# Kernel tuning notes

Measured on AMD Instinct MI355X. Metric: run time of the kernel, lower is better.

Reference implementation:

```python
import jax, jax.numpy as jnp
import numpy as np
import math

STEM = 64
TOK = 128
RADIUS = 0.16
K = 32


def sinusoidal_pos_emb_3d(x, dim):
    # x: [..., 3] -> [..., dim]; dim/3 channels per axis (half sin, half cos)
    per_axis = dim // 3
    half = per_axis // 2
    scale = math.log(10000.0) / (half - 1)
    freqs = jnp.exp(-scale * jnp.arange(half, dtype=x.dtype))  # [half]
    ang = x[..., :, None] * freqs  # [..., 3, half]
    emb = jnp.concatenate([jnp.sin(ang), jnp.cos(ang)], axis=-1)  # [..., 3, per_axis]
    return emb.reshape(*x.shape[:-1], dim)


def query_ball_point(radius, nsample, xyz):
    # xyz: [B, N, 3] -> idx [B, N, nsample] int32
    B, N, _ = xyz.shape
    d2 = jnp.sum((xyz[:, :, None, :] - xyz[:, None, :, :]) ** 2, axis=-1)  # [B,N,N]
    cand = jnp.where(d2 <= radius * radius, jnp.arange(N, dtype=jnp.int32)[None, None, :], N)
    idx = jnp.sort(cand, axis=-1)[..., :nsample]  # first nsample in-ball indices
    first = idx[..., :1]  # self is always in-ball (d=0), so first is valid
    return jnp.where(idx == N, first, idx)


def index_points(points, idx):
    # points [B,N,C], idx [B,S,K] -> [B,S,K,C]
    return jax.vmap(lambda p, i: p[i])(points, idx)


def point_mlp(x, W, b, activate):
    y = x @ W + b
    return jax.nn.relu(y) if activate else y


def setup_inputs() -> dict:
    key = jax.random.key(0)
    ks = jax.random.split(key, 10)
    B, N = 2, 4096
    xyz = jax.random.uniform(ks[0], (B, N, 3), dtype=jnp.float32)
    point_feature = jax.random.normal(ks[1], (B, N, STEM), dtype=jnp.float32)
    c_in = STEM + 3 + 24 + 96  # 187
    def lin(k, i, o):
        s = 1.0 / np.sqrt(i)
        return jax.random.uniform(k, (i, o), jnp.float32, -s, s)
    W1 = lin(ks[2], c_in, TOK); b1 = jnp.zeros((TOK,), jnp.float32)
    W2 = lin(ks[3], TOK, TOK); b2 = jnp.zeros((TOK,), jnp.float32)
    W3 = lin(ks[4], TOK, TOK); b3 = jnp.zeros((TOK,), jnp.float32)
    W4 = lin(ks[5], TOK, TOK); b4 = jnp.zeros((TOK,), jnp.float32)
    return {"xyz": xyz, "point_feature": point_feature,
            "W1": W1, "b1": b1, "W2": W2, "b2": b2,
            "W3": W3, "b3": b3, "W4": W4, "b4": b4}


def reference(xyz, point_feature, W1, b1, W2, b2, W3, b3, W4, b4):
    idx = query_ball_point(RADIUS, K, xyz)                 # [B,N,K]
    grouped_xyz = index_points(xyz, idx)                   # [B,N,K,3]
    grouped_feature = index_points(point_feature, idx)     # [B,N,K,STEM]
    relative_xyz = grouped_xyz - xyz[:, :, None, :]        # [B,N,K,3]
    rel_pe = sinusoidal_pos_emb_3d(relative_xyz, 24)       # [B,N,K,24]
    abs_pe = sinusoidal_pos_emb_3d(xyz, 96)                # [B,N,96]
    abs_pe = jnp.broadcast_to(abs_pe[:, :, None, :], (*idx.shape, 96))
    grouped_input = jnp.concatenate(
        [grouped_feature, relative_xyz, rel_pe, abs_pe], axis=-1)  # [B,N,K,187]
    h = point_mlp(grouped_input, W1, b1, True)
    h = point_mlp(h, W2, b2, False)                        # [B,N,K,TOK]
    scene_point_feature = jnp.max(h, axis=2)               # [B,N,TOK]
    g = jnp.max(scene_point_feature, axis=1, keepdims=True)  # [B,1,TOK]
    g = point_mlp(g, W3, b3, True)
    return point_mlp(g, W4, b4, False)                     # [B,1,TOK]
```

## Files before the change

kernel.cpp:

```cpp
#include <hip/hip_runtime.h>
#include <stdint.h>

#define BATCH 2
#define NPTS  4096
#define KNBR  32
#define TOKC  128

typedef _Float16 half8 __attribute__((ext_vector_type(8)));
typedef _Float16 half4 __attribute__((ext_vector_type(4)));
typedef float    f32x4 __attribute__((ext_vector_type(4)));

#define OFF_FH    (1u << 20)
#define OFF_AH    (3u << 20)
#define OFF_W1F   ((5u << 20) + 2048)
#define OFF_W2F   ((5u << 20) + 10240)
#define OFF_BMAX  (6u << 20)
#define OFF_BMAX2 (7u << 20)
#define OFF_CNT   ((7u << 20) + 32768)

#define NMAIN 1024

__global__ __launch_bounds__(256) void k_pre(const float* __restrict__ xyz,
                                             const float* __restrict__ feat,
                                             const float* __restrict__ W1,
                                             const float* __restrict__ W2,
                                             const float* __restrict__ b1,
                                             int* __restrict__ oidx,
                                             _Float16* __restrict__ Fh,
                                             _Float16* __restrict__ Ah,
                                             _Float16* __restrict__ W1F,
                                             _Float16* __restrict__ W2F,
                                             unsigned int* __restrict__ cntp) {
    __shared__ __align__(16) _Float16 inL[16][168];
    const int t = threadIdx.x;
    const int w = t >> 6, lane = t & 63;

    if (blockIdx.x < 2048) {
        int wave = blockIdx.x * 4 + w;
        int b = wave >> 12;
        int n = wave & (NPTS - 1);
        const float* xb = xyz + (size_t)b * NPTS * 3;
        float cx = xb[n * 3 + 0], cy = xb[n * 3 + 1], cz = xb[n * 3 + 2];
        const float R2 = 0.0256f;
        int cnt = 0;
        int first = 0;
        int* out = oidx + (size_t)wave * KNBR;
        float cur[12], nxt[12];
        #pragma unroll
        for (int u = 0; u < 4; u++) {
            int j = u * 64 + lane;
            cur[u * 3 + 0] = xb[j * 3 + 0];
            cur[u * 3 + 1] = xb[j * 3 + 1];
            cur[u * 3 + 2] = xb[j * 3 + 2];
        }
        for (int base = 0; base < NPTS; base += 256) {
            #pragma clang fp contract(off)
            if (base + 256 < NPTS) {
                #pragma unroll
                for (int u = 0; u < 4; u++) {
                    int j = base + 256 + u * 64 + lane;
                    nxt[u * 3 + 0] = xb[j * 3 + 0];
                    nxt[u * 3 + 1] = xb[j * 3 + 1];
                    nxt[u * 3 + 2] = xb[j * 3 + 2];
                }
            }
            #pragma unroll
            for (int u = 0; u < 4; u++) {
                float dx = cur[u * 3 + 0] - cx, dy = cur[u * 3 + 1] - cy, dz = cur[u * 3 + 2] - cz;
                float d2 = (dx * dx + dy * dy) + dz * dz;
                bool hit = d2 <= R2;
                unsigned long long m = __ballot(hit);
                if (cnt == 0 && m) first = base + u * 64 + (int)__builtin_ctzll(m);
                if (hit) {
                    int pos = cnt + (int)__popcll(m & ((1ull << lane) - 1ull));
                    if (pos < KNBR) out[pos] = base + u * 64 + lane;
                }
                cnt += (int)__popcll(m);
            }
            if (cnt >= KNBR) break;
            #pragma unroll
            for (int i = 0; i < 12; i++) cur[i] = nxt[i];
        }
        if (lane >= cnt && lane < KNBR) out[lane] = first;
        return;
    }

    if (blockIdx.x >= 2560) {
        int f = blockIdx.x - 2560;
        if (f == 0 && t == 0) *cntp = 0u;
        #pragma unroll
        for (int s = 0; s < 2; s++) {
            int e = t + s * 256;
            int ln = e >> 3, j = e & 7;
            int l15 = ln & 15, g = ln >> 4;
            if (f < 8) {
                int k = g * 8 + j;
                int c = f * 16 + l15;
                float val = (k < 27) ? W1[(64 + k) * TOKC + c] : 0.f;
                W1F[f * 512 + e] = (_Float16)val;
            } else {
                int f2 = f - 8;
                int ct = f2 >> 2, kc = f2 & 3;
                int k = kc * 32 + g * 8 + j;
                int c = ct * 16 + l15;
                W2F[f2 * 512 + e] = (_Float16)W2[k * TOKC + c];
            }
        }
        return;
    }

    const int l15 = lane & 15, g = lane >> 4;
    const int g0 = (blockIdx.x - 2048) * 16;

    half8 af[2][2];
    half8 ap[2][3];
    float4 b1v[2];
    #pragma unroll
    for (int rt = 0; rt < 2; rt++) {
        int c = 32 * w + 16 * rt + l15;
        #pragma unroll
        for (int kc = 0; kc < 2; kc++)
            #pragma unroll
            for (int j = 0; j < 8; j++)
                af[rt][kc][j] = (_Float16)W1[(kc * 32 + g * 8 + j) * TOKC + c];
        #pragma unroll
        for (int kc = 0; kc < 3; kc++)
            #pragma unroll
            for (int j = 0; j < 8; j++)
                ap[rt][kc][j] = (_Float16)W1[(91 + kc * 32 + g * 8 + j) * TOKC + c];
        b1v[rt] = *(const float4*)&b1[32 * w + 16 * rt + g * 4];
    }

    {
        float4 v = ((const float4*)(feat + (size_t)g0 * 64))[t];
        half4 hv = {(_Float16)v.x, (_Float16)v.y, (_Float16)v.z, (_Float16)v.w};
        *(half4*)&inL[t >> 4][(t & 15) * 4] = hv;
    }
    {
        int p = t >> 4, v0 = (t & 15) * 6;
        const float* xp = xyz + (size_t)(g0 + p) * 3;
        #pragma unroll
        for (int u = 0; u < 6; u++) {
            int d = v0 + u;
            int a = d >> 5, i = d & 31, fi = i & 15;
            float fr = __expf(-0.6140226914650789f * (float)fi);
            float ang = xp[a] * fr;
            inL[p][64 + d] = (_Float16)((i < 16) ? __sinf(ang) : __cosf(ang));
        }
    }
    __syncthreads();

    f32x4 cF[2], cA[2];
    #pragma unroll
    for (int rt = 0; rt < 2; rt++) { f32x4 z = {0.f, 0.f, 0.f, 0.f}; cF[rt] = z; cA[rt] = z; }
    #pragma unroll
    for (int kc = 0; kc < 2; kc++) {
        half8 bx = *(const half8*)&inL[l15][kc * 32 + g * 8];
        cF[0] = __builtin_amdgcn_mfma_f32_16x16x32_f16(af[0][kc], bx, cF[0], 0, 0, 0);
        cF[1] = __builtin_amdgcn_mfma_f32_16x16x32_f16(af[1][kc], bx, cF[1], 0, 0, 0);
    }
    #pragma unroll
    for (int kc = 0; kc < 3; kc++) {
        half8 bx = *(const half8*)&inL[l15][64 + kc * 32 + g * 8];
        cA[0] = __builtin_amdgcn_mfma_f32_16x16x32_f16(ap[0][kc], bx, cA[0], 0, 0, 0);
        cA[1] = __builtin_amdgcn_mfma_f32_16x16x32_f16(ap[1][kc], bx, cA[1], 0, 0, 0);
    }

    size_t pbase = ((size_t)g0 + l15) * TOKC;
    #pragma unroll
    for (int rt = 0; rt < 2; rt++) {
        int ch0 = 32 * w + 16 * rt + g * 4;
        half4 fv, av;
        #pragma unroll
        for (int r = 0; r < 4; r++) {
            fv[r] = (_Float16)cF[rt][r];
            av[r] = (_Float16)(cA[rt][r] + b1v[rt][r]);
        }
        *(half4*)&Fh[pbase + ch0] = fv;
        *(half4*)&Ah[pbase + ch0] = av;
    }
}

__global__ __launch_bounds__(256, 3) void k_main(const float* __restrict__ xyz,
                                                 const int* __restrict__ idxw,
                                                 const _Float16* __restrict__ Fh,
                                                 const _Float16* __restrict__ Ah,
                                                 const _Float16* __restrict__ W1F,
                                                 const _Float16* __restrict__ W2F,
                                                 float* __restrict__ bmax) {
    __shared__ __align__(16) _Float16 xinL[64 * 40];
    __shared__ __align__(16) _Float16 hfa[64 * 136];
    __shared__ __align__(16) _Float16 arowL[256];
    __shared__ int jidxL[64];

    const int t = threadIdx.x;
    const int w = t >> 6, lane = t & 63;
    const int l15 = lane & 15, g = lane >> 4;
    const int b = blockIdx.x >> 9;
    const int pbase = (blockIdx.x & 511) * 8;
    const float* xb = xyz + (size_t)b * NPTS * 3;

    half8 a1[2];
    half8 a2[2][4];
    #pragma unroll
    for (int rt = 0; rt < 2; rt++) {
        a1[rt] = *(const half8*)&W1F[(2 * w + rt) * 512 + lane * 8];
        #pragma unroll
        for (int kc = 0; kc < 4; kc++)
            a2[rt][kc] = *(const half8*)&W2F[((2 * w + rt) * 4 + kc) * 512 + lane * 8];
    }

    float mxAll[2][4];
    #pragma unroll
    for (int rt = 0; rt < 2; rt++)
        #pragma unroll
        for (int r = 0; r < 4; r++) mxAll[rt][r] = -1e30f;

    const float FR[4] = {1.f, 0.0464158883f, 0.00215443469f, 1e-4f};

    int jreg = 0;
    ushort ar0;
    {
        const size_t gq = (size_t)b * NPTS + pbase;
        if (t < 64) jreg = idxw[gq * KNBR + t];
        ar0 = ((const ushort*)(Ah + gq * TOKC))[t];
    }

    for (int it = 0; it < 4; it++) {
        const int n0 = pbase + it * 2;
        const size_t gp0 = (size_t)b * NPTS + n0;

        if (t < 64) jidxL[t] = jreg;
        ((ushort*)arowL)[t] = ar0;
        __syncthreads();

        if (it < 3) {
            const size_t gq = gp0 + 2;
            if (t < 64) jreg = idxw[gq * KNBR + t];
            ar0 = ((const ushort*)(Ah + gq * TOKC))[t];
        }

        {
            int p = t >> 2, q = t & 3;
            int j = jidxL[p];
            const half8* frp = (const half8*)(Fh + ((size_t)b * NPTS + j) * TOKC + q * 32);
            half8 fb[4];
            #pragma unroll
            for (int i = 0; i < 4; i++) fb[i] = frp[i];
            const half8* arp = (const half8*)(arowL + (p >> 5) * TOKC + q * 32);
            half8* dst = (half8*)(hfa + p * 136 + q * 32);
            #pragma unroll
            for (int i = 0; i < 4; i++) dst[i] = fb[i] + arp[i];
        }
        if (t < 128) {
            int p = t >> 1, hh = t & 1;
            int n = n0 + (p >> 5), j = jidxL[p];
            float rx = xb[j * 3 + 0] - xb[n * 3 + 0];
            float ry = xb[j * 3 + 1] - xb[n * 3 + 1];
            float rz = xb[j * 3 + 2] - xb[n * 3 + 2];
            float v[16];
            if (hh == 0) {
                v[0] = rx; v[1] = ry; v[2] = rz;
                #pragma unroll
                for (int fi = 0; fi < 4; fi++) {
                    float ang = rx * FR[fi];
                    v[3 + fi] = __sinf(ang);
                    v[7 + fi] = __cosf(ang);
                }
                #pragma unroll
                for (int fi = 0; fi < 4; fi++) v[11 + fi] = __sinf(ry * FR[fi]);
                v[15] = __cosf(ry * FR[0]);
            } else {
                #pragma unroll
                for (int fi = 1; fi < 4; fi++) v[fi - 1] = __cosf(ry * FR[fi]);
                #pragma unroll
                for (int fi = 0; fi < 4; fi++) {
                    float ang = rz * FR[fi];
                    v[3 + fi] = __sinf(ang);
                    v[7 + fi] = __cosf(ang);
                }
                #pragma unroll
                for (int i = 11; i < 16; i++) v[i] = 0.f;
            }
            half8 h0, h1;
            #pragma unroll
            for (int i = 0; i < 8; i++) { h0[i] = (_Float16)v[i]; h1[i] = (_Float16)v[8 + i]; }
            *(half8*)&xinL[p * 40 + hh * 16]     = h0;
            *(half8*)&xinL[p * 40 + hh * 16 + 8] = h1;
        }
        __syncthreads();

        #pragma unroll
        for (int ct = 0; ct < 4; ct++) {
            int p = ct * 16 + l15;
            half8 bx = *(const half8*)&xinL[p * 40 + g * 8];
            f32x4 z = {0.f, 0.f, 0.f, 0.f};
            f32x4 c1a = __builtin_amdgcn_mfma_f32_16x16x32_f16(a1[0], bx, z, 0, 0, 0);
            f32x4 c1b = __builtin_amdgcn_mfma_f32_16x16x32_f16(a1[1], bx, z, 0, 0, 0);
            #pragma unroll
            for (int rt = 0; rt < 2; rt++) {
                int ch0 = 32 * w + 16 * rt + g * 4;
                half4* hp = (half4*)&hfa[p * 136 + ch0];
                half4 bias = *hp;
                f32x4 cc = rt ? c1b : c1a;
                half4 hv;
                #pragma unroll
                for (int r = 0; r < 4; r++) {
                    float s = cc[r] + (float)bias[r];
                    hv[r] = (_Float16)fmaxf(s, 0.f);
                }
                *hp = hv;
            }
        }
        __syncthreads();

        f32x4 c2[4][2];
        #pragma unroll
        for (int ct = 0; ct < 4; ct++)
            #pragma unroll
            for (int rt = 0; rt < 2; rt++) {
                f32x4 z = {0.f, 0.f, 0.f, 0.f};
                c2[ct][rt] = z;
            }
        #pragma unroll
        for (int kc = 0; kc < 4; kc++) {
            #pragma unroll
            for (int ct = 0; ct < 4; ct++) {
                half8 bx = *(const half8*)&hfa[(ct * 16 + l15) * 136 + kc * 32 + g * 8];
                c2[ct][0] = __builtin_amdgcn_mfma_f32_16x16x32_f16(a2[0][kc], bx, c2[ct][0], 0, 0, 0);
                c2[ct][1] = __builtin_amdgcn_mfma_f32_16x16x32_f16(a2[1][kc], bx, c2[ct][1], 0, 0, 0);
            }
        }
        #pragma unroll
        for (int rt = 0; rt < 2; rt++)
            #pragma unroll
            for (int r = 0; r < 4; r++) {
                float m0 = fmaxf(fmaxf(c2[0][rt][r], c2[1][rt][r]), fmaxf(c2[2][rt][r], c2[3][rt][r]));
                mxAll[rt][r] = fmaxf(mxAll[rt][r], m0);
            }
        __syncthreads();
    }

    #pragma unroll
    for (int rt = 0; rt < 2; rt++)
        #pragma unroll
        for (int r = 0; r < 4; r++)
            #pragma unroll
            for (int off = 1; off < 16; off <<= 1)
                mxAll[rt][r] = fmaxf(mxAll[rt][r], __shfl_xor(mxAll[rt][r], off));

    if (l15 == 0) {
        float* brow = bmax + (size_t)blockIdx.x * TOKC;
        float4 v0 = make_float4(mxAll[0][0], mxAll[0][1], mxAll[0][2], mxAll[0][3]);
        float4 v1 = make_float4(mxAll[1][0], mxAll[1][1], mxAll[1][2], mxAll[1][3]);
        *(float4*)&brow[32 * w + g * 4]      = v0;
        *(float4*)&brow[32 * w + 16 + g * 4] = v1;
    }
}

__global__ __launch_bounds__(256) void k_redtail(const float* __restrict__ bmax,
                                                 float* __restrict__ bmax2,
                                                 unsigned int* __restrict__ cntp,
                                                 const float* __restrict__ b2,
                                                 const float* __restrict__ W3,
                                                 const float* __restrict__ b3,
                                                 const float* __restrict__ W4,
                                                 const float* __restrict__ b4,
                                                 float* __restrict__ out) {
    __shared__ float red[256];
    __shared__ float gl[256], sl[256];
    __shared__ unsigned int lastFlag;
    const int i = blockIdx.x, t = threadIdx.x;
    const int c = t & 127, h = t >> 7;
    {
        const float* base = bmax + ((size_t)i * 16 + (size_t)h * 8) * TOKC + c;
        float m = -1e30f;
        #pragma unroll
        for (int k = 0; k < 8; k++) m = fmaxf(m, base[(size_t)k * TOKC]);
        red[t] = m;
    }
    __syncthreads();
    if (t < 128) bmax2[(size_t)i * TOKC + t] = fmaxf(red[t], red[t + 128]);
    __threadfence();
    __syncthreads();
    if (t == 0) lastFlag = (atomicAdd(cntp, 1u) == 63u) ? 1u : 0u;
    __syncthreads();
    if (!lastFlag) return;

    const int bb = h;
    {
        unsigned int* bp = (unsigned int*)bmax2 + (size_t)bb * 32 * TOKC + c;
        float m = -1e30f;
        #pragma unroll
        for (int k = 0; k < 32; k++) {
            unsigned int u = atomicOr(&bp[(size_t)k * TOKC], 0u);
            m = fmaxf(m, __uint_as_float(u));
        }
        gl[t] = m + b2[c];
    }
    __syncthreads();
    {
        float s = b3[c];
        for (int k = 0; k < 128; k++) s += gl[bb * 128 + k] * W3[k * TOKC + c];
        sl[t] = fmaxf(s, 0.f);
    }
    __syncthreads();
    {
        float o = b4[c];
        for (int k = 0; k < 128; k++) o += sl[bb * 128 + k] * W4[k * TOKC + c];
        out[t] = o;
    }
}

extern "C" void kernel_launch(void* const* d_in, const int* in_sizes, int n_in,
                              void* d_out, int out_size, void* d_ws, size_t ws_size,
                              hipStream_t stream) {
    const float* xyz  = (const float*)d_in[0];
    const float* feat = (const float*)d_in[1];
    const float* W1   = (const float*)d_in[2];
    const float* b1   = (const float*)d_in[3];
    const float* W2   = (const float*)d_in[4];
    const float* b2   = (const float*)d_in[5];
    const float* W3   = (const float*)d_in[6];
    const float* b3   = (const float*)d_in[7];
    const float* W4   = (const float*)d_in[8];
    const float* b4   = (const float*)d_in[9];

    char* ws = (char*)d_ws;
    int*          idxw  = (int*)ws;
    _Float16*     Fh    = (_Float16*)(ws + OFF_FH);
    _Float16*     Ah    = (_Float16*)(ws + OFF_AH);
    _Float16*     W1F   = (_Float16*)(ws + OFF_W1F);
    _Float16*     W2F   = (_Float16*)(ws + OFF_W2F);
    float*        bmax  = (float*)(ws + OFF_BMAX);
    float*        bmax2 = (float*)(ws + OFF_BMAX2);
    unsigned int* cntp  = (unsigned int*)(ws + OFF_CNT);

    k_pre<<<dim3(2600), dim3(256), 0, stream>>>(xyz, feat, W1, W2, b1,
                                                idxw, Fh, Ah, W1F, W2F, cntp);
    k_main<<<dim3(NMAIN), dim3(256), 0, stream>>>(xyz, idxw, Fh, Ah, W1F, W2F, bmax);
    k_redtail<<<dim3(64), dim3(256), 0, stream>>>(bmax, bmax2, cntp,
                                                  b2, W3, b3, W4, b4, (float*)d_out);
}
```

Before: 125.4 us.

## Add prep kernel for SoA coordinates and pre-packed fp16 W1 fragments

```diff
diff --git a/kernel.cpp b/kernel.cpp
--- a/kernel.cpp
+++ b/kernel.cpp
@@ -14,33 +14,82 @@
 #define OFF_AH    (3u << 20)
 #define OFF_W1F   ((5u << 20) + 2048)
 #define OFF_W2F   ((5u << 20) + 10240)
+#define OFF_W1FA  ((5u << 20) + 43008)
+#define OFF_W1FP  ((5u << 20) + 59392)
+#define OFF_SOA   ((5u << 20) + 83968)
 #define OFF_BMAX  (6u << 20)
 #define OFF_BMAX2 (7u << 20)
 #define OFF_CNT   ((7u << 20) + 32768)
 
 #define NMAIN 1024
 
+__global__ __launch_bounds__(256) void k_soa(const float* __restrict__ xyz,
+                                             const float* __restrict__ W1,
+                                             const float* __restrict__ W2,
+                                             float* __restrict__ soa,
+                                             _Float16* __restrict__ W1F,
+                                             _Float16* __restrict__ W2F,
+                                             _Float16* __restrict__ W1FA,
+                                             _Float16* __restrict__ W1FP,
+                                             unsigned int* __restrict__ cntp) {
+    const int t = threadIdx.x;
+    if (blockIdx.x < 32) {
+        int p = blockIdx.x * 256 + t;
+        float x = xyz[p * 3 + 0], y = xyz[p * 3 + 1], z = xyz[p * 3 + 2];
+        float* xs = soa;
+        float* ys = soa + 8192;
+        float* zs = soa + 16384;
+        xs[p] = x; ys[p] = y; zs[p] = z;
+        if (blockIdx.x == 0 && t == 0) *cntp = 0u;
+        return;
+    }
+    int f = blockIdx.x - 32;
+    #pragma unroll
+    for (int s = 0; s < 2; s++) {
+        int e = t + s * 256;
+        int ln = e >> 3, j = e & 7;
+        int l15 = ln & 15, g = ln >> 4;
+        if (f < 8) {
+            int k = g * 8 + j;
+            int c = f * 16 + l15;
+            W1F[f * 512 + e] = (_Float16)((k < 27) ? W1[(64 + k) * TOKC + c] : 0.f);
+        } else if (f < 40) {
+            int f2 = f - 8;
+            int ct = f2 >> 2, kc = f2 & 3;
+            W2F[f2 * 512 + e] = (_Float16)W2[(kc * 32 + g * 8 + j) * TOKC + ct * 16 + l15];
+        } else if (f < 56) {
+            int f3 = f - 40;
+            int tile = f3 >> 1, kc = f3 & 1;
+            W1FA[f3 * 512 + e] = (_Float16)W1[(kc * 32 + g * 8 + j) * TOKC + tile * 16 + l15];
+        } else {
+            int f4 = f - 56;
+            int tile = f4 / 3, kc = f4 % 3;
+            W1FP[f4 * 512 + e] = (_Float16)W1[(91 + kc * 32 + g * 8 + j) * TOKC + tile * 16 + l15];
+        }
+    }
+}
+
 __global__ __launch_bounds__(256) void k_pre(const float* __restrict__ xyz,
                                              const float* __restrict__ feat,
-                                             const float* __restrict__ W1,
-                                             const float* __restrict__ W2,
                                              const float* __restrict__ b1,
+                                             const float* __restrict__ soa,
+                                             const _Float16* __restrict__ W1FA,
+                                             const _Float16* __restrict__ W1FP,
                                              int* __restrict__ oidx,
                                              _Float16* __restrict__ Fh,
-                                             _Float16* __restrict__ Ah,
-                                             _Float16* __restrict__ W1F,
-                                             _Float16* __restrict__ W2F,
-                                             unsigned int* __restrict__ cntp) {
+                                             _Float16* __restrict__ Ah) {
     __shared__ __align__(16) _Float16 inL[16][168];
     const int t = threadIdx.x;
     const int w = t >> 6, lane = t & 63;
 
-    if (blockIdx.x < 2048) {
-        int wave = blockIdx.x * 4 + w;
+    if (blockIdx.x >= 512) {
+        int wave = (blockIdx.x - 512) * 4 + w;
         int b = wave >> 12;
         int n = wave & (NPTS - 1);
-        const float* xb = xyz + (size_t)b * NPTS * 3;
-        float cx = xb[n * 3 + 0], cy = xb[n * 3 + 1], cz = xb[n * 3 + 2];
+        const float* xs = soa + (size_t)b * NPTS;
+        const float* ys = soa + 8192 + (size_t)b * NPTS;
+        const float* zs = soa + 16384 + (size_t)b * NPTS;
+        float cx = xs[n], cy = ys[n], cz = zs[n];
         const float R2 = 0.0256f;
         int cnt = 0;
         int first = 0;
@@ -49,9 +98,7 @@
         #pragma unroll
         for (int u = 0; u < 4; u++) {
             int j = u * 64 + lane;
-            cur[u * 3 + 0] = xb[j * 3 + 0];
-            cur[u * 3 + 1] = xb[j * 3 + 1];
-            cur[u * 3 + 2] = xb[j * 3 + 2];
+            cur[u * 3 + 0] = xs[j]; cur[u * 3 + 1] = ys[j]; cur[u * 3 + 2] = zs[j];
         }
         for (int base = 0; base < NPTS; base += 256) {
             #pragma clang fp contract(off)
@@ -59,9 +106,7 @@
                 #pragma unroll
                 for (int u = 0; u < 4; u++) {
                     int j = base + 256 + u * 64 + lane;
-                    nxt[u * 3 + 0] = xb[j * 3 + 0];
-                    nxt[u * 3 + 1] = xb[j * 3 + 1];
-                    nxt[u * 3 + 2] = xb[j * 3 + 2];
+                    nxt[u * 3 + 0] = xs[j]; nxt[u * 3 + 1] = ys[j]; nxt[u * 3 + 2] = zs[j];
                 }
             }
             #pragma unroll
@@ -85,49 +130,20 @@
         return;
     }
 
-    if (blockIdx.x >= 2560) {
-        int f = blockIdx.x - 2560;
-        if (f == 0 && t == 0) *cntp = 0u;
-        #pragma unroll
-        for (int s = 0; s < 2; s++) {
-            int e = t + s * 256;
-            int ln = e >> 3, j = e & 7;
-            int l15 = ln & 15, g = ln >> 4;
-            if (f < 8) {
-                int k = g * 8 + j;
-                int c = f * 16 + l15;
-                float val = (k < 27) ? W1[(64 + k) * TOKC + c] : 0.f;
-                W1F[f * 512 + e] = (_Float16)val;
-            } else {
-                int f2 = f - 8;
-                int ct = f2 >> 2, kc = f2 & 3;
-                int k = kc * 32 + g * 8 + j;
-                int c = ct * 16 + l15;
-                W2F[f2 * 512 + e] = (_Float16)W2[k * TOKC + c];
-            }
-        }
-        return;
-    }
-
     const int l15 = lane & 15, g = lane >> 4;
-    const int g0 = (blockIdx.x - 2048) * 16;
+    const int g0 = blockIdx.x * 16;
 
     half8 af[2][2];
     half8 ap[2][3];
     float4 b1v[2];
     #pragma unroll
     for (int rt = 0; rt < 2; rt++) {
-        int c = 32 * w + 16 * rt + l15;
         #pragma unroll
         for (int kc = 0; kc < 2; kc++)
-            #pragma unroll
-            for (int j = 0; j < 8; j++)
-                af[rt][kc][j] = (_Float16)W1[(kc * 32 + g * 8 + j) * TOKC + c];
+            af[rt][kc] = *(const half8*)&W1FA[(((2 * w + rt) * 2 + kc)) * 512 + lane * 8];
         #pragma unroll
         for (int kc = 0; kc < 3; kc++)
-            #pragma unroll
-            for (int j = 0; j < 8; j++)
-                ap[rt][kc][j] = (_Float16)W1[(91 + kc * 32 + g * 8 + j) * TOKC + c];
+            ap[rt][kc] = *(const half8*)&W1FP[(((2 * w + rt) * 3 + kc)) * 512 + lane * 8];
         b1v[rt] = *(const float4*)&b1[32 * w + 16 * rt + g * 4];
     }
 
@@ -432,12 +448,15 @@
     _Float16*     Ah    = (_Float16*)(ws + OFF_AH);
     _Float16*     W1F   = (_Float16*)(ws + OFF_W1F);
     _Float16*     W2F   = (_Float16*)(ws + OFF_W2F);
+    _Float16*     W1FA  = (_Float16*)(ws + OFF_W1FA);
+    _Float16*     W1FP  = (_Float16*)(ws + OFF_W1FP);
+    float*        soa   = (float*)(ws + OFF_SOA);
     float*        bmax  = (float*)(ws + OFF_BMAX);
     float*        bmax2 = (float*)(ws + OFF_BMAX2);
     unsigned int* cntp  = (unsigned int*)(ws + OFF_CNT);
 
-    k_pre<<<dim3(2600), dim3(256), 0, stream>>>(xyz, feat, W1, W2, b1,
-                                                idxw, Fh, Ah, W1F, W2F, cntp);
+    k_soa<<<dim3(112), dim3(256), 0, stream>>>(xyz, W1, W2, soa, W1F, W2F, W1FA, W1FP, cntp);
+    k_pre<<<dim3(2560), dim3(256), 0, stream>>>(xyz, feat, b1, soa, W1FA, W1FP, idxw, Fh, Ah);
     k_main<<<dim3(NMAIN), dim3(256), 0, stream>>>(xyz, idxw, Fh, Ah, W1F, W2F, bmax);
     k_redtail<<<dim3(64), dim3(256), 0, stream>>>(bmax, bmax2, cntp,
                                                   b2, W3, b3, W4, b4, (float*)d_out);
```

Result: slower. 131.0 us (+4.5%).
